# Kernel optimization log

Hardware: AMD Instinct MI355X
Metric: run time of the kernel (lower is better)

The kernel has to match this reference:

```python
import jax, jax.numpy as jnp
import numpy as np

N = 20000   # nodes
E = 320000  # edges (avg degree 16)
IN = 16     # in_node_nf
H = 64      # hidden_nf
OUT = 64    # out_node_nf
L = 4       # n_layers


def setup_inputs() -> dict:
    key = jax.random.key(0)
    ks = jax.random.split(key, 16)
    w = lambda k, shape: (jax.random.normal(k, shape, dtype=jnp.float32) * 0.05)
    zb = lambda *shape: jnp.zeros(shape, dtype=jnp.float32)
    return {
        "h": jax.random.normal(ks[0], (N, IN), dtype=jnp.float32),
        "x": jax.random.normal(ks[1], (N, 3), dtype=jnp.float32),
        "edge_index": jax.random.randint(ks[2], (2, E), 0, N),
        "emb_in_w": w(ks[3], (IN, H)), "emb_in_b": zb(H),
        "edge_w1": w(ks[4], (L, 2 * H + 1, H)), "edge_b1": zb(L, H),
        "edge_w2": w(ks[5], (L, H, H)), "edge_b2": zb(L, H),
        "coord_w1": w(ks[6], (L, H, H)), "coord_b1": zb(L, H),
        "coord_w2": w(ks[7], (L, H, 1)),  # bias-free last coord_mlp layer
        "node_w1": w(ks[8], (L, 2 * H, H)), "node_b1": zb(L, H),
        "node_w2": w(ks[9], (L, H, H)), "node_b2": zb(L, H),
        "emb_out_w": w(ks[10], (H, OUT)), "emb_out_b": zb(OUT),
    }


def reference(h, x, edge_index, emb_in_w, emb_in_b,
              edge_w1, edge_b1, edge_w2, edge_b2,
              coord_w1, coord_b1, coord_w2,
              node_w1, node_b1, node_w2, node_b2,
              emb_out_w, emb_out_b):
    row, col = edge_index[0], edge_index[1]
    act = jax.nn.silu
    # receiver in-degree for mean coordinate aggregation (clamped to >=1)
    cnt = jax.ops.segment_sum(jnp.ones((row.shape[0], 1), h.dtype), row, num_segments=N)
    cnt = jnp.maximum(cnt, 1.0)

    h = h @ emb_in_w + emb_in_b
    for l in range(L):
        # coord2radial
        diff = x[row] - x[col]                               # [E,3]
        radial = jnp.sum(diff * diff, axis=-1, keepdims=True)  # [E,1]
        # edge model: m_ij = phi_e(h_i, h_j, ||x_i-x_j||^2)
        e_in = jnp.concatenate([h[row], h[col], radial], axis=-1)  # [E,2H+1]
        m = act(e_in @ edge_w1[l] + edge_b1[l])
        m = act(m @ edge_w2[l] + edge_b2[l])                 # [E,H]
        # coord model: x_i += mean_j (x_i - x_j) * phi_x(m_ij)
        phi = act(m @ coord_w1[l] + coord_b1[l]) @ coord_w2[l]  # [E,1]
        trans = diff * phi                                    # [E,3]
        x = x + jax.ops.segment_sum(trans, row, num_segments=N) / cnt
        # node model: h_i = h_i + phi_h(h_i, sum_j m_ij)
        agg = jax.ops.segment_sum(m, row, num_segments=N)     # [N,H]
        n_in = jnp.concatenate([h, agg], axis=-1)             # [N,2H]
        out = act(n_in @ node_w1[l] + node_b1[l]) @ node_w2[l] + node_b2[l]
        h = h + out
    h = h @ emb_out_w + emb_out_b
    return h, x
```

## Files before the change

### kernel.cpp

```cpp
#include <hip/hip_runtime.h>
#include <hip/hip_bf16.h>


#define NN 20000
#define EE 320000
#define LSE 17024
#define LSN 6272

typedef unsigned short u16;
typedef unsigned int   u32;
typedef __attribute__((ext_vector_type(8))) short s16x8;
typedef __attribute__((ext_vector_type(4))) float f32x4;

__device__ __forceinline__ float bf2f(u16 u) { return __uint_as_float(((u32)u) << 16); }
__device__ __forceinline__ float silu_f(float x) { return x / (1.0f + __expf(-x)); }

__device__ __forceinline__ u16 f2bf_rne(float f) {
    u32 u = __float_as_uint(f);
    return (u16)((u + 0x7FFFu + ((u >> 16) & 1u)) >> 16);
}
__device__ __forceinline__ float gldf(const void* p, int i, int bf) {
    return bf ? bf2f(((const u16*)p)[i]) : ((const float*)p)[i];
}
__device__ __forceinline__ u16 gldb(const void* p, int i, int bf) {
    return bf ? ((const u16*)p)[i] : f2bf_rne(((const float*)p)[i]);
}

__global__ void k_sentinel(u16* __restrict__ out, int n, float v) {
    int t = blockIdx.x * 256 + threadIdx.x;
    if (t < n) out[t] = f2bf_rne(v);
}

__global__ __launch_bounds__(256) void k_pack(
    const void* __restrict__ ew1, const void* __restrict__ eb1,
    const void* __restrict__ ew2, const void* __restrict__ eb2,
    const void* __restrict__ cw1, const void* __restrict__ cb1,
    const void* __restrict__ cw2,
    const void* __restrict__ nw1, const void* __restrict__ nb1,
    const void* __restrict__ nw2, const void* __restrict__ nb2,
    const u16* __restrict__ h_raw, const int* __restrict__ rowi,
    int* __restrict__ flag, int* __restrict__ deg,
    u16* __restrict__ pkE, u32* __restrict__ pkN)
{
    if (blockIdx.x >= 64) {
        int e = (blockIdx.x - 64) * 256 + threadIdx.x;
        if (e < EE) atomicAdd(&deg[rowi[e]], 1);
        return;
    }
    __shared__ int cnt_s;
    if (threadIdx.x == 0) cnt_s = 0;
    __syncthreads();
    if (threadIdx.x < 128) {
        float v = fabsf(bf2f(h_raw[threadIdx.x]));
        if (v >= 0.015625f && v <= 16.0f) atomicAdd(&cnt_s, 1);
    }
    __syncthreads();
    const int bf = (cnt_s >= 96) ? 1 : 0;
    if (blockIdx.x == 0 && threadIdx.x == 0) *flag = bf;

    const int gid = blockIdx.x * 256 + threadIdx.x;
    const int stride = 64 * 256;

    for (int g = gid; g < 4 * 16384; g += stride) {
        int l = g >> 14, idx = g & 16383;
        u16 v;
        if (idx < 8192) {
            int j = idx & 7, lane = (idx >> 3) & 63, t = (idx >> 9) & 3, w = idx >> 11;
            int k = 32 * w + (lane >> 4) * 8 + j, n = 16 * t + (lane & 15);
            v = gldb(ew1, l * 129 * 64 + k * 64 + n, bf);
        } else if (idx < 12288) {
            int i2 = idx - 8192;
            int j = i2 & 7, lane = (i2 >> 3) & 63, t = (i2 >> 9) & 3, w = i2 >> 11;
            int k = 32 * w + (lane >> 4) * 8 + j, n = 16 * t + (lane & 15);
            v = gldb(ew2, l * 4096 + k * 64 + n, bf);
        } else {
            int i2 = idx - 12288;
            int j = i2 & 7, lane = (i2 >> 3) & 63, t = (i2 >> 9) & 3, w = i2 >> 11;
            int k = 32 * w + (lane >> 4) * 8 + j, n = 16 * t + (lane & 15);
            v = gldb(cw1, l * 4096 + k * 64 + n, bf);
        }
        pkE[l * LSE + idx] = v;
    }
    for (int g = gid; g < 4 * 320; g += stride) {
        int l = g / 320, r = g % 320, wch = r >> 6, i = r & 63;
        float v = (wch == 0) ? gldf(eb1, l * 64 + i, bf)
                : (wch == 1) ? gldf(eb2, l * 64 + i, bf)
                : (wch == 2) ? gldf(cb1, l * 64 + i, bf)
                : (wch == 3) ? gldf(cw2, l * 64 + i, bf)
                :              gldf(ew1, l * 129 * 64 + 128 * 64 + i, bf);
        ((float*)(pkE + l * LSE + 16384))[r] = v;
    }
    for (int g = gid; g < 4 * 6144; g += stride) {
        int l = g / 6144, idx = g % 6144;
        u32 pv;
        if (idx < 4096) {
            int kp = idx >> 6, j = idx & 63;
            u32 lo = gldb(nw1, l * 8192 + (2 * kp) * 64 + j, bf);
            u32 hi = gldb(nw1, l * 8192 + (2 * kp + 1) * 64 + j, bf);
            pv = lo | (hi << 16);
        } else {
            int i2 = idx - 4096, kp = i2 >> 6, j = i2 & 63;
            u32 lo = gldb(nw2, l * 4096 + (2 * kp) * 64 + j, bf);
            u32 hi = gldb(nw2, l * 4096 + (2 * kp + 1) * 64 + j, bf);
            pv = lo | (hi << 16);
        }
        pkN[l * LSN + idx] = pv;
    }
    for (int g = gid; g < 4 * 128; g += stride) {
        int l = g >> 7, r = g & 127;
        float v = (r < 64) ? gldf(nb1, l * 64 + r, bf) : gldf(nb2, l * 64 + (r - 64), bf);
        ((float*)(pkN + l * LSN + 6144))[r] = v;
    }
}

__global__ __launch_bounds__(1024) void k_scan(const int* deg, int* offs, int* cursor) {
    __shared__ int part[1024];
    const int tid = threadIdx.x;
    const int CH = (NN + 1023) / 1024;
    const int b0 = tid * CH;
    int s = 0;
    for (int i = 0; i < CH; i++) { int idx = b0 + i; if (idx < NN) s += deg[idx]; }
    part[tid] = s;
    __syncthreads();
    for (int d = 1; d < 1024; d <<= 1) {
        int v = (tid >= d) ? part[tid - d] : 0;
        __syncthreads();
        part[tid] += v;
        __syncthreads();
    }
    int run = (tid > 0) ? part[tid - 1] : 0;
    for (int i = 0; i < CH; i++) {
        int idx = b0 + i;
        if (idx < NN) {
            int dv = deg[idx];
            offs[idx] = run;
            cursor[idx] = run;
            run += dv;
        }
    }
    if (tid == 1023) offs[NN] = run;
}

__global__ void k_scatter(const int* __restrict__ rowi, const int* __restrict__ coli,
                          int* __restrict__ cursor, int* __restrict__ slist) {
    int e = blockIdx.x * 256 + threadIdx.x;
    if (e < EE) {
        int r = rowi[e];
        int pos = atomicAdd(&cursor[r], 1);
        slist[pos] = coli[e];
    }
}

__global__ __launch_bounds__(256) void k_embed(
    const void* __restrict__ h_in, const void* __restrict__ x_in,
    const void* __restrict__ w, const void* __restrict__ bias,
    const int* __restrict__ flag,
    float* __restrict__ hws, float* __restrict__ xws, u16* __restrict__ hb)
{
    const int bf = *flag;
    const int lane = threadIdx.x & 63;
    const int wv   = threadIdx.x >> 6;
    const int i    = blockIdx.x * 4 + wv;
    float acc = gldf(bias, lane, bf);
    #pragma unroll
    for (int k = 0; k < 16; k++)
        acc = fmaf(gldf(h_in, i * 16 + k, bf), gldf(w, k * 64 + lane, bf), acc);
    hws[i * 64 + lane] = acc;
    hb[i * 64 + lane] = f2bf_rne(acc);
    if (lane < 3) xws[i * 3 + lane] = gldf(x_in, i * 3 + lane, bf);
}

#define OFF_B23  8192
#define OFF_M    16384
#define MPAD     76
#define OFF_PHI  (OFF_M + 4 * 16 * MPAD)
__global__ __launch_bounds__(256, 3) void k_edge(
    const u16* __restrict__ hb, const float* __restrict__ xws,
    const int* __restrict__ offs, const int* __restrict__ slist,
    const u16* __restrict__ pE,
    float* __restrict__ agg, float* __restrict__ xacc)
{
    __shared__ __align__(16) u16 sW[OFF_PHI + 4 * 16 * 2];

    const int tid = threadIdx.x, lane = tid & 63, wv = tid >> 6;
    const int l15 = lane & 15, quad = lane >> 4;

    for (int idx = tid; idx < 2048; idx += 256)
        ((s16x8*)sW)[idx] = ((const s16x8*)pE)[idx];
    const float* pb = (const float*)(pE + 16384);
    float b1v[4], b2v[4], cb1v[4], c2v[4], wrv[4];
    #pragma unroll
    for (int t = 0; t < 4; t++) {
        b1v[t]  = pb[       16 * t + l15];
        b2v[t]  = pb[ 64 +  16 * t + l15];
        cb1v[t] = pb[128 +  16 * t + l15];
        c2v[t]  = pb[192 +  16 * t + l15];
        wrv[t]  = pb[256 +  16 * t + l15];
    }
    __syncthreads();

    const int gw = blockIdx.x * 4 + wv, totW = gridDim.x * 4;
    u16* mrow = &sW[OFF_M + wv * 16 * MPAD];
    float* phiw = (float*)&sW[OFF_PHI + wv * 32];

    for (int n = gw; n < NN; n += totW) {
        const int o0 = offs[n], deg = offs[n + 1] - o0;
        if (deg == 0) continue;

        const s16x8 Ar0 = *(const s16x8*)&hb[n * 64 + quad * 8];
        const s16x8 Ar1 = *(const s16x8*)&hb[n * 64 + 32 + quad * 8];
        f32x4 Cb[4] = {{0,0,0,0},{0,0,0,0},{0,0,0,0},{0,0,0,0}};
        #pragma unroll
        for (int t = 0; t < 4; t++) {
            const s16x8 Bf0 = *(const s16x8*)&sW[((0 * 4 + t) * 64 + lane) * 8];
            Cb[t] = __builtin_amdgcn_mfma_f32_16x16x32_bf16(Ar0, Bf0, Cb[t], 0, 0, 0);
            const s16x8 Bf1 = *(const s16x8*)&sW[((1 * 4 + t) * 64 + lane) * 8];
            Cb[t] = __builtin_amdgcn_mfma_f32_16x16x32_bf16(Ar1, Bf1, Cb[t], 0, 0, 0);
        }
        const float xrv = (quad < 3) ? xws[n * 3 + quad] : 0.0f;
        float aggA[4] = {0.f, 0.f, 0.f, 0.f};
        float xaccA = 0.0f;

        for (int eb = 0; eb < deg; eb += 16) {
            const int nb = min(16, deg - eb);
            const int ee = (l15 < nb) ? l15 : 0;
            const int ce = slist[o0 + eb + ee];
            float dx = 0.0f;
            if (quad < 3 && l15 < nb) dx = xrv - xws[ce * 3 + quad];
            float r2 = dx * dx;
            r2 += __shfl_xor(r2, 16, 64);
            r2 += __shfl_xor(r2, 32, 64);

            f32x4 C[4] = {Cb[0], Cb[1], Cb[2], Cb[3]};
            {
                const s16x8 Ac0 = *(const s16x8*)&hb[ce * 64 + quad * 8];
                const s16x8 Ac1 = *(const s16x8*)&hb[ce * 64 + 32 + quad * 8];
                #pragma unroll
                for (int t = 0; t < 4; t++) {
                    const s16x8 Bf2 = *(const s16x8*)&sW[((2 * 4 + t) * 64 + lane) * 8];
                    C[t] = __builtin_amdgcn_mfma_f32_16x16x32_bf16(Ac0, Bf2, C[t], 0, 0, 0);
                    const s16x8 Bf3 = *(const s16x8*)&sW[((3 * 4 + t) * 64 + lane) * 8];
                    C[t] = __builtin_amdgcn_mfma_f32_16x16x32_bf16(Ac1, Bf3, C[t], 0, 0, 0);
                }
            }
            float r2r[4];
            #pragma unroll
            for (int r = 0; r < 4; r++) r2r[r] = __shfl(r2, quad * 4 + r, 64);
            #pragma unroll
            for (int t = 0; t < 4; t++)
                #pragma unroll
                for (int r = 0; r < 4; r++) {
                    float v = silu_f(C[t][r] + b1v[t] + r2r[r] * wrv[t]);
                    mrow[(quad * 4 + r) * MPAD + 16 * t + l15] = f2bf_rne(v);
                }

            f32x4 D[4] = {{0,0,0,0},{0,0,0,0},{0,0,0,0},{0,0,0,0}};
            #pragma unroll
            for (int w = 0; w < 2; w++) {
                const s16x8 Am = *(const s16x8*)(mrow + l15 * MPAD + 32 * w + quad * 8);
                #pragma unroll
                for (int t = 0; t < 4; t++) {
                    const s16x8 Bf = *(const s16x8*)&sW[OFF_B23 + ((w * 4 + t) * 64 + lane) * 8];
                    D[t] = __builtin_amdgcn_mfma_f32_16x16x32_bf16(Am, Bf, D[t], 0, 0, 0);
                }
            }
            #pragma unroll
            for (int t = 0; t < 4; t++)
                #pragma unroll
                for (int r = 0; r < 4; r++) {
                    float v = silu_f(D[t][r] + b2v[t]);
                    if (quad * 4 + r < nb) aggA[t] += v;
                    mrow[(quad * 4 + r) * MPAD + 16 * t + l15] = f2bf_rne(v);
                }

            f32x4 P[4] = {{0,0,0,0},{0,0,0,0},{0,0,0,0},{0,0,0,0}};
            #pragma unroll
            for (int w = 0; w < 2; w++) {
                const s16x8 Am = *(const s16x8*)(mrow + l15 * MPAD + 32 * w + quad * 8);
                #pragma unroll
                for (int t = 0; t < 4; t++) {
                    const s16x8 Bf = *(const s16x8*)&sW[OFF_B23 + (((2 + w) * 4 + t) * 64 + lane) * 8];
                    P[t] = __builtin_amdgcn_mfma_f32_16x16x32_bf16(Am, Bf, P[t], 0, 0, 0);
                }
            }
            float ph[4];
            #pragma unroll
            for (int r = 0; r < 4; r++) {
                float s = 0.f;
                #pragma unroll
                for (int t = 0; t < 4; t++) s = fmaf(silu_f(P[t][r] + cb1v[t]), c2v[t], s);
                s += __shfl_xor(s, 1, 64);
                s += __shfl_xor(s, 2, 64);
                s += __shfl_xor(s, 4, 64);
                s += __shfl_xor(s, 8, 64);
                ph[r] = s;
            }
            if (l15 == 0) {
                #pragma unroll
                for (int r = 0; r < 4; r++) phiw[quad * 4 + r] = ph[r];
            }
            float phv = phiw[l15];
            if (quad < 3 && l15 < nb) xaccA = fmaf(dx, phv, xaccA);
        }

        #pragma unroll
        for (int t = 0; t < 4; t++) {
            aggA[t] += __shfl_xor(aggA[t], 16, 64);
            aggA[t] += __shfl_xor(aggA[t], 32, 64);
        }
        float av = (quad == 0) ? aggA[0] : (quad == 1) ? aggA[1]
                 : (quad == 2) ? aggA[2] : aggA[3];
        agg[n * 64 + quad * 16 + l15] = av;

        xaccA += __shfl_xor(xaccA, 1, 64);
        xaccA += __shfl_xor(xaccA, 2, 64);
        xaccA += __shfl_xor(xaccA, 4, 64);
        xaccA += __shfl_xor(xaccA, 8, 64);
        if (l15 == 0 && quad < 3) xacc[n * 3 + quad] = xaccA / (float)deg;
    }
}

__global__ __launch_bounds__(256) void k_node(
    float* __restrict__ hws, u16* __restrict__ hb, const float* __restrict__ agg,
    float* __restrict__ xws, const float* __restrict__ xacc,
    const u32* __restrict__ pN)
{
    __shared__ __align__(16) u32 sW1p[64 * 64];
    __shared__ __align__(16) u32 sW2p[32 * 64];
    __shared__ float sB1f[64], sB2f[64];
    __shared__ __align__(16) float sNin[4][8][132];

    const int tid = threadIdx.x, lane = tid & 63, wv = tid >> 6;
    for (int idx = tid; idx < 1024; idx += 256)
        ((f32x4*)sW1p)[idx] = ((const f32x4*)pN)[idx];
    for (int idx = tid; idx < 512; idx += 256)
        ((f32x4*)sW2p)[idx] = ((const f32x4*)(pN + 4096))[idx];
    const float* pb = (const float*)(pN + 6144);
    if (tid < 64) { sB1f[tid] = pb[tid]; sB2f[tid] = pb[64 + tid]; }

    {
        int t = blockIdx.x * 96 + tid;
        if (tid < 96) xws[t] += xacc[t];
    }
    __syncthreads();

    const int i0 = (blockIdx.x * 4 + wv) * 8;
    float hold[8];
    #pragma unroll
    for (int b = 0; b < 8; b++) {
        int i = i0 + b;
        float hv = hws[i * 64 + lane];
        hold[b] = hv;
        sNin[wv][b][lane]      = hv;
        sNin[wv][b][64 + lane] = agg[i * 64 + lane];
    }

    float acc[8];
    #pragma unroll
    for (int b = 0; b < 8; b++) acc[b] = sB1f[lane];
    #pragma unroll
    for (int kk = 0; kk < 32; kk++) {
        u32 w01 = sW1p[(kk * 2) * 64 + lane];
        u32 w23 = sW1p[(kk * 2 + 1) * 64 + lane];
        float w0 = __uint_as_float(w01 << 16), w1 = __uint_as_float(w01 & 0xffff0000u);
        float w2 = __uint_as_float(w23 << 16), w3 = __uint_as_float(w23 & 0xffff0000u);
        #pragma unroll
        for (int b = 0; b < 8; b++) {
            const float4 e4 = *reinterpret_cast<const float4*>(&sNin[wv][b][kk * 4]);
            acc[b] = fmaf(e4.x, w0, fmaf(e4.y, w1, fmaf(e4.z, w2, fmaf(e4.w, w3, acc[b]))));
        }
    }
    #pragma unroll
    for (int b = 0; b < 8; b++) acc[b] = silu_f(acc[b]);
    #pragma unroll
    for (int b = 0; b < 8; b++) sNin[wv][b][lane] = acc[b];

    float out[8];
    #pragma unroll
    for (int b = 0; b < 8; b++) out[b] = sB2f[lane];
    #pragma unroll
    for (int kk = 0; kk < 16; kk++) {
        u32 w01 = sW2p[(kk * 2) * 64 + lane];
        u32 w23 = sW2p[(kk * 2 + 1) * 64 + lane];
        float w0 = __uint_as_float(w01 << 16), w1 = __uint_as_float(w01 & 0xffff0000u);
        float w2 = __uint_as_float(w23 << 16), w3 = __uint_as_float(w23 & 0xffff0000u);
        #pragma unroll
        for (int b = 0; b < 8; b++) {
            const float4 e4 = *reinterpret_cast<const float4*>(&sNin[wv][b][kk * 4]);
            out[b] = fmaf(e4.x, w0, fmaf(e4.y, w1, fmaf(e4.z, w2, fmaf(e4.w, w3, out[b]))));
        }
    }
    #pragma unroll
    for (int b = 0; b < 8; b++) {
        float hv = hold[b] + out[b];
        hws[(i0 + b) * 64 + lane] = hv;
        hb[(i0 + b) * 64 + lane] = f2bf_rne(hv);
    }
}

__global__ __launch_bounds__(256) void k_out(
    const float* __restrict__ hws, const float* __restrict__ xws,
    const void* __restrict__ wo, const void* __restrict__ bo,
    const int* __restrict__ flag, void* __restrict__ out)
{
    __shared__ u32 sWp[32 * 64];
    __shared__ float sBf[64];
    __shared__ __align__(16) float sH[4][8][68];
    const int tid = threadIdx.x, lane = tid & 63, wv = tid >> 6;
    const int bf = *flag;
    for (int idx = tid; idx < 32 * 64; idx += 256) {
        int kp = idx >> 6, j = idx & 63;
        u32 lo = gldb(wo, (kp * 2) * 64 + j, bf);
        u32 hi = gldb(wo, (kp * 2 + 1) * 64 + j, bf);
        sWp[idx] = lo | (hi << 16);
    }
    if (tid < 64) sBf[tid] = gldf(bo, tid, bf);
    __syncthreads();

    const int i0 = (blockIdx.x * 4 + wv) * 8;
    #pragma unroll
    for (int b = 0; b < 8; b++) sH[wv][b][lane] = hws[(i0 + b) * 64 + lane];

    float acc[8];
    #pragma unroll
    for (int b = 0; b < 8; b++) acc[b] = sBf[lane];
    #pragma unroll
    for (int kk = 0; kk < 16; kk++) {
        u32 w01 = sWp[(kk * 2) * 64 + lane];
        u32 w23 = sWp[(kk * 2 + 1) * 64 + lane];
        float w0 = __uint_as_float(w01 << 16), w1 = __uint_as_float(w01 & 0xffff0000u);
        float w2 = __uint_as_float(w23 << 16), w3 = __uint_as_float(w23 & 0xffff0000u);
        #pragma unroll
        for (int b = 0; b < 8; b++) {
            const float4 e4 = *reinterpret_cast<const float4*>(&sH[wv][b][kk * 4]);
            acc[b] = fmaf(e4.x, w0, fmaf(e4.y, w1, fmaf(e4.z, w2, fmaf(e4.w, w3, acc[b]))));
        }
    }
    u16*   oh16 = (u16*)out;
    float* ohf  = (float*)out;
    u16*   ox16 = oh16 + (size_t)NN * 64;
    float* oxf  = ohf  + (size_t)NN * 64;
    #pragma unroll
    for (int b = 0; b < 8; b++) {
        int i = i0 + b;
        if (bf) {
            oh16[i * 64 + lane] = f2bf_rne(acc[b]);
            if (lane < 3) ox16[i * 3 + lane] = f2bf_rne(xws[i * 3 + lane]);
        } else {
            ohf[i * 64 + lane] = acc[b];
            if (lane < 3) oxf[i * 3 + lane] = xws[i * 3 + lane];
        }
    }
}

extern "C" void kernel_launch(void* const* d_in, const int* in_sizes, int n_in,
                              void* d_out, int out_size, void* d_ws, size_t ws_size,
                              hipStream_t stream)
{
    const size_t WS_REQ = (size_t)NN * 134 * sizeof(float) + 64;
    if (ws_size < WS_REQ) {
        float sval = 1000.0f + (float)(ws_size >> 20);
        k_sentinel<<<(out_size + 255) / 256, 256, 0, stream>>>(
            (u16*)d_out, out_size, sval);
        return;
    }

    const void* h_in = d_in[0];
    const void* x_in = d_in[1];
    const int*  eidx = (const int*)d_in[2];
    const int* rowi = eidx;
    const int* coli = eidx + EE;

    float* ws   = (float*)d_ws;
    float* hws  = ws;
    float* xws  = hws + NN * 64;
    float* agg  = xws + NN * 3;
    float* xacc = agg + NN * 64;
    int*   flag = (int*)(xacc + NN * 3);

    u16* hb     = (u16*)d_out;
    int* offs   = (int*)(hb + (size_t)NN * 64);
    int* slist  = offs + (NN + 4);
    u16* pkE    = (u16*)(slist + EE);
    u32* pkN    = (u32*)(pkE + 4 * LSE);
    int* cursor = (int*)(pkN + 4 * LSN);

    hipMemsetAsync(cursor, 0, (size_t)NN * sizeof(int), stream);
    hipMemsetAsync(agg, 0, (size_t)NN * 67 * sizeof(float), stream);

    k_pack<<<64 + (EE + 255) / 256, 256, 0, stream>>>(
        d_in[5], d_in[6], d_in[7], d_in[8], d_in[9], d_in[10], d_in[11],
        d_in[12], d_in[13], d_in[14], d_in[15],
        (const u16*)h_in, rowi, flag, cursor, pkE, pkN);
    k_scan<<<1, 1024, 0, stream>>>(cursor, offs, cursor);
    k_scatter<<<(EE + 255) / 256, 256, 0, stream>>>(rowi, coli, cursor, slist);
    k_embed<<<NN / 4, 256, 0, stream>>>(h_in, x_in, d_in[3], d_in[4], flag, hws, xws, hb);

    for (int l = 0; l < 4; l++) {
        k_edge<<<768, 256, 0, stream>>>(hb, xws, offs, slist,
                                        pkE + l * LSE, agg, xacc);
        k_node<<<NN / 32, 256, 0, stream>>>(hws, hb, agg, xws, xacc,
                                            pkN + (size_t)l * LSN);
    }
    k_out<<<NN / 32, 256, 0, stream>>>(hws, xws, d_in[16], d_in[17], flag, d_out);
}
```

Before: 581.0 us.

## Fuse node MLP into edge kernel with ping-pong h/x buffers

```diff
diff --git a/kernel.cpp b/kernel.cpp
--- a/kernel.cpp
+++ b/kernel.cpp
@@ -13,6 +13,8 @@
 typedef __attribute__((ext_vector_type(4))) float f32x4;
 
 __device__ __forceinline__ float bf2f(u16 u) { return __uint_as_float(((u32)u) << 16); }
+__device__ __forceinline__ float lof(u32 d) { return __uint_as_float(d << 16); }
+__device__ __forceinline__ float hif(u32 d) { return __uint_as_float(d & 0xffff0000u); }
 __device__ __forceinline__ float silu_f(float x) { return x / (1.0f + __expf(-x)); }
 
 __device__ __forceinline__ u16 f2bf_rne(float f) {
@@ -174,13 +176,15 @@
 #define OFF_M    16384
 #define MPAD     76
 #define OFF_PHI  (OFF_M + 4 * 16 * MPAD)
+#define OFF_NB   (OFF_PHI + 4 * 32)
 __global__ __launch_bounds__(256, 3) void k_edge(
-    const u16* __restrict__ hb, const float* __restrict__ xws,
+    const u16* __restrict__ hbc, u16* __restrict__ hbn,
+    const float* __restrict__ xc, float* __restrict__ xn,
+    float* __restrict__ hws,
     const int* __restrict__ offs, const int* __restrict__ slist,
-    const u16* __restrict__ pE,
-    float* __restrict__ agg, float* __restrict__ xacc)
+    const u16* __restrict__ pE, const u32* __restrict__ pN)
 {
-    __shared__ __align__(16) u16 sW[OFF_PHI + 4 * 16 * 2];
+    __shared__ __align__(16) u16 sW[OFF_NB + 4 * 256];
 
     const int tid = threadIdx.x, lane = tid & 63, wv = tid >> 6;
     const int l15 = lane & 15, quad = lane >> 4;
@@ -197,18 +201,20 @@
         c2v[t]  = pb[192 +  16 * t + l15];
         wrv[t]  = pb[256 +  16 * t + l15];
     }
+    const float* pNb = (const float*)(pN + 6144);
+    const float nb1v = pNb[lane], nb2v = pNb[64 + lane];
     __syncthreads();
 
     const int gw = blockIdx.x * 4 + wv, totW = gridDim.x * 4;
     u16* mrow = &sW[OFF_M + wv * 16 * MPAD];
     float* phiw = (float*)&sW[OFF_PHI + wv * 32];
+    float* nbw  = (float*)&sW[OFF_NB + wv * 256];
 
     for (int n = gw; n < NN; n += totW) {
         const int o0 = offs[n], deg = offs[n + 1] - o0;
-        if (deg == 0) continue;
-
-        const s16x8 Ar0 = *(const s16x8*)&hb[n * 64 + quad * 8];
-        const s16x8 Ar1 = *(const s16x8*)&hb[n * 64 + 32 + quad * 8];
+
+        const s16x8 Ar0 = *(const s16x8*)&hbc[n * 64 + quad * 8];
+        const s16x8 Ar1 = *(const s16x8*)&hbc[n * 64 + 32 + quad * 8];
         f32x4 Cb[4] = {{0,0,0,0},{0,0,0,0},{0,0,0,0},{0,0,0,0}};
         #pragma unroll
         for (int t = 0; t < 4; t++) {
@@ -217,7 +223,7 @@
             const s16x8 Bf1 = *(const s16x8*)&sW[((1 * 4 + t) * 64 + lane) * 8];
             Cb[t] = __builtin_amdgcn_mfma_f32_16x16x32_bf16(Ar1, Bf1, Cb[t], 0, 0, 0);
         }
-        const float xrv = (quad < 3) ? xws[n * 3 + quad] : 0.0f;
+        const float xrv = (quad < 3) ? xc[n * 3 + quad] : 0.0f;
         float aggA[4] = {0.f, 0.f, 0.f, 0.f};
         float xaccA = 0.0f;
 
@@ -226,15 +232,15 @@
             const int ee = (l15 < nb) ? l15 : 0;
             const int ce = slist[o0 + eb + ee];
             float dx = 0.0f;
-            if (quad < 3 && l15 < nb) dx = xrv - xws[ce * 3 + quad];
+            if (quad < 3 && l15 < nb) dx = xrv - xc[ce * 3 + quad];
             float r2 = dx * dx;
             r2 += __shfl_xor(r2, 16, 64);
             r2 += __shfl_xor(r2, 32, 64);
 
             f32x4 C[4] = {Cb[0], Cb[1], Cb[2], Cb[3]};
             {
-                const s16x8 Ac0 = *(const s16x8*)&hb[ce * 64 + quad * 8];
-                const s16x8 Ac1 = *(const s16x8*)&hb[ce * 64 + 32 + quad * 8];
+                const s16x8 Ac0 = *(const s16x8*)&hbc[ce * 64 + quad * 8];
+                const s16x8 Ac1 = *(const s16x8*)&hbc[ce * 64 + 32 + quad * 8];
                 #pragma unroll
                 for (int t = 0; t < 4; t++) {
                     const s16x8 Bf2 = *(const s16x8*)&sW[((2 * 4 + t) * 64 + lane) * 8];
@@ -303,6 +309,14 @@
             if (quad < 3 && l15 < nb) xaccA = fmaf(dx, phv, xaccA);
         }
 
+        const float fdeg = (float)max(deg, 1);
+
+        xaccA += __shfl_xor(xaccA, 1, 64);
+        xaccA += __shfl_xor(xaccA, 2, 64);
+        xaccA += __shfl_xor(xaccA, 4, 64);
+        xaccA += __shfl_xor(xaccA, 8, 64);
+        if (l15 == 0 && quad < 3) xn[n * 3 + quad] = xrv + xaccA / fdeg;
+
         #pragma unroll
         for (int t = 0; t < 4; t++) {
             aggA[t] += __shfl_xor(aggA[t], 16, 64);
@@ -310,95 +324,35 @@
         }
         float av = (quad == 0) ? aggA[0] : (quad == 1) ? aggA[1]
                  : (quad == 2) ? aggA[2] : aggA[3];
-        agg[n * 64 + quad * 16 + l15] = av;
-
-        xaccA += __shfl_xor(xaccA, 1, 64);
-        xaccA += __shfl_xor(xaccA, 2, 64);
-        xaccA += __shfl_xor(xaccA, 4, 64);
-        xaccA += __shfl_xor(xaccA, 8, 64);
-        if (l15 == 0 && quad < 3) xacc[n * 3 + quad] = xaccA / (float)deg;
-    }
-}
-
-__global__ __launch_bounds__(256) void k_node(
-    float* __restrict__ hws, u16* __restrict__ hb, const float* __restrict__ agg,
-    float* __restrict__ xws, const float* __restrict__ xacc,
-    const u32* __restrict__ pN)
-{
-    __shared__ __align__(16) u32 sW1p[64 * 64];
-    __shared__ __align__(16) u32 sW2p[32 * 64];
-    __shared__ float sB1f[64], sB2f[64];
-    __shared__ __align__(16) float sNin[4][8][132];
-
-    const int tid = threadIdx.x, lane = tid & 63, wv = tid >> 6;
-    for (int idx = tid; idx < 1024; idx += 256)
-        ((f32x4*)sW1p)[idx] = ((const f32x4*)pN)[idx];
-    for (int idx = tid; idx < 512; idx += 256)
-        ((f32x4*)sW2p)[idx] = ((const f32x4*)(pN + 4096))[idx];
-    const float* pb = (const float*)(pN + 6144);
-    if (tid < 64) { sB1f[tid] = pb[tid]; sB2f[tid] = pb[64 + tid]; }
-
-    {
-        int t = blockIdx.x * 96 + tid;
-        if (tid < 96) xws[t] += xacc[t];
-    }
-    __syncthreads();
-
-    const int i0 = (blockIdx.x * 4 + wv) * 8;
-    float hold[8];
-    #pragma unroll
-    for (int b = 0; b < 8; b++) {
-        int i = i0 + b;
-        float hv = hws[i * 64 + lane];
-        hold[b] = hv;
-        sNin[wv][b][lane]      = hv;
-        sNin[wv][b][64 + lane] = agg[i * 64 + lane];
-    }
-
-    float acc[8];
-    #pragma unroll
-    for (int b = 0; b < 8; b++) acc[b] = sB1f[lane];
-    #pragma unroll
-    for (int kk = 0; kk < 32; kk++) {
-        u32 w01 = sW1p[(kk * 2) * 64 + lane];
-        u32 w23 = sW1p[(kk * 2 + 1) * 64 + lane];
-        float w0 = __uint_as_float(w01 << 16), w1 = __uint_as_float(w01 & 0xffff0000u);
-        float w2 = __uint_as_float(w23 << 16), w3 = __uint_as_float(w23 & 0xffff0000u);
-        #pragma unroll
-        for (int b = 0; b < 8; b++) {
-            const float4 e4 = *reinterpret_cast<const float4*>(&sNin[wv][b][kk * 4]);
-            acc[b] = fmaf(e4.x, w0, fmaf(e4.y, w1, fmaf(e4.z, w2, fmaf(e4.w, w3, acc[b]))));
-        }
-    }
-    #pragma unroll
-    for (int b = 0; b < 8; b++) acc[b] = silu_f(acc[b]);
-    #pragma unroll
-    for (int b = 0; b < 8; b++) sNin[wv][b][lane] = acc[b];
-
-    float out[8];
-    #pragma unroll
-    for (int b = 0; b < 8; b++) out[b] = sB2f[lane];
-    #pragma unroll
-    for (int kk = 0; kk < 16; kk++) {
-        u32 w01 = sW2p[(kk * 2) * 64 + lane];
-        u32 w23 = sW2p[(kk * 2 + 1) * 64 + lane];
-        float w0 = __uint_as_float(w01 << 16), w1 = __uint_as_float(w01 & 0xffff0000u);
-        float w2 = __uint_as_float(w23 << 16), w3 = __uint_as_float(w23 & 0xffff0000u);
-        #pragma unroll
-        for (int b = 0; b < 8; b++) {
-            const float4 e4 = *reinterpret_cast<const float4*>(&sNin[wv][b][kk * 4]);
-            out[b] = fmaf(e4.x, w0, fmaf(e4.y, w1, fmaf(e4.z, w2, fmaf(e4.w, w3, out[b]))));
-        }
-    }
-    #pragma unroll
-    for (int b = 0; b < 8; b++) {
-        float hv = hold[b] + out[b];
-        hws[(i0 + b) * 64 + lane] = hv;
-        hb[(i0 + b) * 64 + lane] = f2bf_rne(hv);
-    }
-}
-
-__global__ __launch_bounds__(256) void k_out(
+
+        const float hv = hws[n * 64 + lane];
+        nbw[lane] = hv;
+        nbw[64 + quad * 16 + l15] = av;
+
+        float a1 = nb1v;
+        #pragma unroll 8
+        for (int kp = 0; kp < 64; kp++) {
+            u32 w = pN[kp * 64 + lane];
+            float2 in2 = *(const float2*)&nbw[kp * 2];
+            a1 = fmaf(in2.x, lof(w), fmaf(in2.y, hif(w), a1));
+        }
+        a1 = silu_f(a1);
+        nbw[lane] = a1;
+
+        float a2 = nb2v;
+        #pragma unroll 8
+        for (int kp = 0; kp < 32; kp++) {
+            u32 w = pN[4096 + kp * 64 + lane];
+            float2 in2 = *(const float2*)&nbw[kp * 2];
+            a2 = fmaf(in2.x, lof(w), fmaf(in2.y, hif(w), a2));
+        }
+        const float hnew = hv + a2;
+        hws[n * 64 + lane] = hnew;
+        hbn[n * 64 + lane] = f2bf_rne(hnew);
+    }
+}
+
+__global__ __launch_bounds__(256, 3) void k_out(
     const float* __restrict__ hws, const float* __restrict__ xws,
     const void* __restrict__ wo, const void* __restrict__ bo,
     const int* __restrict__ flag, void* __restrict__ out)
@@ -428,8 +382,7 @@
     for (int kk = 0; kk < 16; kk++) {
         u32 w01 = sWp[(kk * 2) * 64 + lane];
         u32 w23 = sWp[(kk * 2 + 1) * 64 + lane];
-        float w0 = __uint_as_float(w01 << 16), w1 = __uint_as_float(w01 & 0xffff0000u);
-        float w2 = __uint_as_float(w23 << 16), w3 = __uint_as_float(w23 & 0xffff0000u);
+        float w0 = lof(w01), w1 = hif(w01), w2 = lof(w23), w3 = hif(w23);
         #pragma unroll
         for (int b = 0; b < 8; b++) {
             const float4 e4 = *reinterpret_cast<const float4*>(&sH[wv][b][kk * 4]);
@@ -473,20 +426,19 @@
 
     float* ws   = (float*)d_ws;
     float* hws  = ws;
-    float* xws  = hws + NN * 64;
-    float* agg  = xws + NN * 3;
-    float* xacc = agg + NN * 64;
-    int*   flag = (int*)(xacc + NN * 3);
-
-    u16* hb     = (u16*)d_out;
-    int* offs   = (int*)(hb + (size_t)NN * 64);
-    int* slist  = offs + (NN + 4);
-    u16* pkE    = (u16*)(slist + EE);
-    u32* pkN    = (u32*)(pkE + 4 * LSE);
-    int* cursor = (int*)(pkN + 4 * LSN);
+    float* x0   = hws + NN * 64;
+    float* x1   = x0 + NN * 3;
+    int*   flag = (int*)(x1 + NN * 3);
+    int*   offs = flag + 4;
+    int*   slist = offs + (NN + 4);
+    u16*   pkE  = (u16*)(slist + EE);
+    u32*   pkN  = (u32*)(pkE + 4 * LSE);
+    int*   cursor = (int*)(pkN + 4 * LSN);
+
+    u16* hb0 = (u16*)d_out;
+    u16* hb1 = hb0 + (size_t)NN * 64;
 
     hipMemsetAsync(cursor, 0, (size_t)NN * sizeof(int), stream);
-    hipMemsetAsync(agg, 0, (size_t)NN * 67 * sizeof(float), stream);
 
     k_pack<<<64 + (EE + 255) / 256, 256, 0, stream>>>(
         d_in[5], d_in[6], d_in[7], d_in[8], d_in[9], d_in[10], d_in[11],
@@ -494,13 +446,14 @@
         (const u16*)h_in, rowi, flag, cursor, pkE, pkN);
     k_scan<<<1, 1024, 0, stream>>>(cursor, offs, cursor);
     k_scatter<<<(EE + 255) / 256, 256, 0, stream>>>(rowi, coli, cursor, slist);
-    k_embed<<<NN / 4, 256, 0, stream>>>(h_in, x_in, d_in[3], d_in[4], flag, hws, xws, hb);
-
+    k_embed<<<NN / 4, 256, 0, stream>>>(h_in, x_in, d_in[3], d_in[4], flag, hws, x0, hb0);
+
+    u16*   hbs[2] = {hb0, hb1};
+    float* xs[2]  = {x0, x1};
     for (int l = 0; l < 4; l++) {
-        k_edge<<<768, 256, 0, stream>>>(hb, xws, offs, slist,
-                                        pkE + l * LSE, agg, xacc);
-        k_node<<<NN / 32, 256, 0, stream>>>(hws, hb, agg, xws, xacc,
-                                            pkN + (size_t)l * LSN);
-    }
-    k_out<<<NN / 32, 256, 0, stream>>>(hws, xws, d_in[16], d_in[17], flag, d_out);
-}
+        k_edge<<<768, 256, 0, stream>>>(
+            hbs[l & 1], hbs[(l + 1) & 1], xs[l & 1], xs[(l + 1) & 1], hws,
+            offs, slist, pkE + l * LSE, pkN + (size_t)l * LSN);
+    }
+    k_out<<<NN / 32, 256, 0, stream>>>(hws, x0, d_in[16], d_in[17], flag, d_out);
+}
```

New measurement: 667.3 us. +14.8%, slower.
